# Performance work log

Measured on AMD Instinct MI355X. Metric: run time of the kernel, lower is better.

## Reference

```python
import jax, jax.numpy as jnp
import numpy as np

B, S, H = 4, 2048, 1024
NH = 16
D = H // NH
SCALE = 1.0 / np.sqrt(D).astype(np.float32)


def setup_inputs() -> dict:
    key = jax.random.key(0)
    ks = jax.random.split(key, 5)
    s = 1.0 / np.sqrt(H).astype(np.float32)  # ~ torch Linear init scale
    return {
        "x": jax.random.normal(ks[0], (B, S, H), jnp.float32),
        "Wq": jax.random.normal(ks[1], (H, H), jnp.float32) * s,
        "bq": jnp.zeros((H,), jnp.float32),
        "Wk": jax.random.normal(ks[2], (H, H), jnp.float32) * s,
        "bk": jnp.zeros((H,), jnp.float32),
        "Wv": jax.random.normal(ks[3], (H, H), jnp.float32) * s,
        "bv": jnp.zeros((H,), jnp.float32),
        "Wo": jax.random.normal(ks[4], (H, H), jnp.float32) * s,
        "bo": jnp.zeros((H,), jnp.float32),
    }


def reference(x, Wq, bq, Wk, bk, Wv, bv, Wo, bo):
    b, s, h = x.shape
    # qkv projections, split into heads: [b, nh, s, d]
    q = (x @ Wq.T + bq).reshape(b, s, NH, D).transpose(0, 2, 1, 3)
    k = (x @ Wk.T + bk).reshape(b, s, NH, D).transpose(0, 2, 1, 3)
    v = (x @ Wv.T + bv).reshape(b, s, NH, D).transpose(0, 2, 1, 3)
    att = jnp.einsum("bhqd,bhkd->bhqk", q, k) * SCALE
    att = jax.nn.softmax(att, axis=-1)  # stable max-subtract softmax
    # dropout(p=0.5) is identity in eval mode
    out = jnp.einsum("bhqk,bhkd->bhqd", att, v)
    out = out.transpose(0, 2, 1, 3).reshape(b, s, h)
    return out @ Wo.T + bo
```

## Files before the change

### kernel.cpp

```cpp
#include <hip/hip_runtime.h>
#include <hip/hip_bf16.h>
#include <stdint.h>
#include <math.h>

#define NB 4
#define NS 2048
#define NHID 1024
#define NHEAD 16
#define ND 64
#define NM (NB * NS)

typedef unsigned short u16;
typedef __attribute__((ext_vector_type(8))) short bf16x8;
typedef __attribute__((ext_vector_type(4))) float f32x4;

#define SC2F 0.18033688011112042f
#define DEFER_T 11.5416f


__device__ __forceinline__ u16 f2bf(float f) {
  union { float f; unsigned u; } v; v.f = f;
  unsigned u = v.u;
  return (u16)((u + 0x7FFFu + ((u >> 16) & 1u)) >> 16);
}

__device__ __forceinline__ void gload_lds16(const u16* g, u16* l) {
  __builtin_amdgcn_global_load_lds(
      (const __attribute__((address_space(1))) void*)g,
      (__attribute__((address_space(3))) void*)l, 16, 0, 0);
}

__device__ __forceinline__ f32x4 mfma16(bf16x8 a, bf16x8 b, f32x4 c) {
  return __builtin_amdgcn_mfma_f32_16x16x32_bf16(a, b, c, 0, 0, 0);
}

__device__ __forceinline__ unsigned cvtpk(float lo, float hi) {
  unsigned d;
  asm("v_cvt_pk_bf16_f32 %0, %1, %2" : "=v"(d) : "v"(lo), "v"(hi));
  return d;
}


__global__ __launch_bounds__(256) void convert_f32_bf16(
    const float* __restrict__ x, const float* __restrict__ wq,
    const float* __restrict__ wk, const float* __restrict__ wv,
    const float* __restrict__ wo,
    u16* __restrict__ xb, u16* __restrict__ wqb, u16* __restrict__ wkb,
    u16* __restrict__ wvb, u16* __restrict__ wob) {
  const float* src; u16* dst; int n;
  switch (blockIdx.y) {
    case 0:  src = x;  dst = xb;  n = NM * NHID;   break;
    case 1:  src = wq; dst = wqb; n = NHID * NHID; break;
    case 2:  src = wk; dst = wkb; n = NHID * NHID; break;
    case 3:  src = wv; dst = wvb; n = NHID * NHID; break;
    default: src = wo; dst = wob; n = NHID * NHID; break;
  }
  int stride = gridDim.x * blockDim.x * 4;
  for (int i = (blockIdx.x * blockDim.x + threadIdx.x) * 4; i < n; i += stride) {
    float4 v = *reinterpret_cast<const float4*>(src + i);
    ushort4 o;
    o.x = f2bf(v.x); o.y = f2bf(v.y); o.z = f2bf(v.z); o.w = f2bf(v.w);
    *reinterpret_cast<ushort4*>(dst + i) = o;
  }
}


__device__ __forceinline__ void gemm128_mainloop(
    const u16* __restrict__ A, const u16* __restrict__ Bw, int Kdim,
    int bm, int bn, u16* As, u16* Bs, f32x4 (&acc)[4][4]) {
  const int t = threadIdx.x;
  const int w = t >> 6;
  const int l = t & 63;
  const int lr = l & 15;
  const int kh = l >> 4;
  const int wr = w >> 1, wc = w & 1;

#pragma unroll
  for (int mi = 0; mi < 4; ++mi)
#pragma unroll
    for (int ni = 0; ni < 4; ++ni) acc[mi][ni] = (f32x4){0.f, 0.f, 0.f, 0.f};

  for (int k0 = 0; k0 < Kdim; k0 += 32) {
    __syncthreads();
#pragma unroll
    for (int j = 0; j < 2; ++j) {
      int idx = j * 256 + t;
      int row = idx >> 2;
      int kk  = (idx & 3) << 3;
      gload_lds16(A  + (size_t)(bm + row) * Kdim + k0 + kk, As + (size_t)(j * 256 + w * 64) * 8);
      gload_lds16(Bw + (size_t)(bn + row) * Kdim + k0 + kk, Bs + (size_t)(j * 256 + w * 64) * 8);
    }
    __syncthreads();

    bf16x8 af[4], bfr[4];
#pragma unroll
    for (int mi = 0; mi < 4; ++mi)
      af[mi] = *(const bf16x8*)&As[(wr * 64 + mi * 16 + lr) * 32 + kh * 8];
#pragma unroll
    for (int ni = 0; ni < 4; ++ni)
      bfr[ni] = *(const bf16x8*)&Bs[(wc * 64 + ni * 16 + lr) * 32 + kh * 8];
#pragma unroll
    for (int mi = 0; mi < 4; ++mi)
#pragma unroll
      for (int ni = 0; ni < 4; ++ni)
        acc[mi][ni] = mfma16(af[mi], bfr[ni], acc[mi][ni]);
  }
}


__global__ __launch_bounds__(256) void gemm_qkv(
    const u16* __restrict__ xb,
    const u16* __restrict__ wqb, const u16* __restrict__ wkb, const u16* __restrict__ wvb,
    const float* __restrict__ bq, const float* __restrict__ bk, const float* __restrict__ bv,
    u16* __restrict__ Qo, u16* __restrict__ Ko, u16* __restrict__ Vo) {
  __shared__ __align__(16) u16 As[128 * 32];
  __shared__ __align__(16) u16 Bs[128 * 32];
  const int which = blockIdx.z;
  const u16* Bw = (which == 0) ? wqb : (which == 1) ? wkb : wvb;
  const float* bias = (which == 0) ? bq : (which == 1) ? bk : bv;
  u16* outp = (which == 0) ? Qo : (which == 1) ? Ko : Vo;
  const int bm = blockIdx.x * 128, bn = blockIdx.y * 128;

  f32x4 acc[4][4];
  gemm128_mainloop(xb, Bw, NHID, bm, bn, As, Bs, acc);

  const int t = threadIdx.x, w = t >> 6, l = t & 63, lr = l & 15, hr = l >> 4;
  const int wr = w >> 1, wc = w & 1;
#pragma unroll
  for (int mi = 0; mi < 4; ++mi)
#pragma unroll
    for (int ni = 0; ni < 4; ++ni)
#pragma unroll
      for (int r = 0; r < 4; ++r) {
        int m = bm + wr * 64 + mi * 16 + hr * 4 + r;
        int n = bn + wc * 64 + ni * 16 + lr;
        float v = acc[mi][ni][r] + bias[n];
        if (which == 0) v *= SC2F;
        int b = m >> 11, s = m & (NS - 1), h = n >> 6, d = n & (ND - 1);
        size_t addr;
        if (which < 2) {
          addr = (((size_t)(b * NHEAD + h)) * NS + s) * ND + d;
        } else {
          int sp = (s & ~31) | (((s >> 2) & 3) * 8 + ((s >> 4) & 1) * 4 + (s & 3));
          addr = (((size_t)(b * NHEAD + h)) * ND + d) * NS + sp;
        }
        outp[addr] = f2bf(v);
      }
}


__global__ __launch_bounds__(256, 4) void attn_kernel(
    const u16* __restrict__ Q, const u16* __restrict__ K,
    const u16* __restrict__ Vt, u16* __restrict__ AO) {
  __shared__ __align__(16) u16 Ks[2][64 * 64];
  __shared__ __align__(16) u16 Vs[2][64 * 64];

  const int t = threadIdx.x, w = t >> 6, l = t & 63;
  const int lr = l & 15, g = l >> 4;
  const int bh = blockIdx.y;
  const int q0 = blockIdx.x * 128;

  const u16* Qh = Q  + (size_t)bh * NS * ND;
  const u16* Kh = K  + (size_t)bh * NS * ND;
  const u16* Vh = Vt + (size_t)bh * NS * ND;

  bf16x8 qf[2][2];
#pragma unroll
  for (int mi = 0; mi < 2; ++mi)
#pragma unroll
    for (int ks = 0; ks < 2; ++ks)
      qf[mi][ks] = *(const bf16x8*)(Qh + (size_t)(q0 + w * 32 + mi * 16 + lr) * ND + ks * 32 + g * 8);

  auto stage_kv = [&](int kt, int b) {
#pragma unroll
    for (int j = 0; j < 2; ++j) {
      int idx = j * 256 + t;
      int row = idx >> 3, sch = (idx & 7) ^ (row & 7);
      gload_lds16(Kh + (size_t)(kt + row) * ND + sch * 8, Ks[b] + (size_t)(j * 256 + w * 64) * 8);
      gload_lds16(Vh + (size_t)row * NS + kt + sch * 8,   Vs[b] + (size_t)(j * 256 + w * 64) * 8);
    }
  };

  stage_kv(0, 0);
  stage_kv(64, 1);

  f32x4 o[2][4];
  float m_i[2], l_i[2];
#pragma unroll
  for (int mi = 0; mi < 2; ++mi) {
#pragma unroll
    for (int ni = 0; ni < 4; ++ni) o[mi][ni] = (f32x4){0.f, 0.f, 0.f, 0.f};
    m_i[mi] = -INFINITY; l_i[mi] = 0.f;
  }

  const int nt = NS / 64;
  for (int ti = 0; ti < nt; ++ti) {
    const int b = ti & 1;
    if (ti == nt - 1) asm volatile("s_waitcnt vmcnt(0)" ::: "memory");
    else              asm volatile("s_waitcnt vmcnt(4)" ::: "memory");
    __builtin_amdgcn_s_barrier();

    f32x4 s[2][4];
#pragma unroll
    for (int mi = 0; mi < 2; ++mi)
#pragma unroll
      for (int ni = 0; ni < 4; ++ni) s[mi][ni] = (f32x4){0.f, 0.f, 0.f, 0.f};
    __builtin_amdgcn_s_setprio(1);
#pragma unroll
    for (int ks = 0; ks < 2; ++ks)
#pragma unroll
      for (int ni = 0; ni < 4; ++ni) {
        bf16x8 kf = *(const bf16x8*)&Ks[b][(ni * 16 + lr) * 64 + ((ks * 4 + g) ^ (lr & 7)) * 8];
        s[0][ni] = mfma16(kf, qf[0][ks], s[0][ni]);
        s[1][ni] = mfma16(kf, qf[1][ks], s[1][ni]);
      }
    __builtin_amdgcn_s_setprio(0);

    float pm[2];
#pragma unroll
    for (int mi = 0; mi < 2; ++mi) {
      float a0 = fmaxf(fmaxf(s[mi][0][0], s[mi][0][1]), fmaxf(s[mi][0][2], s[mi][0][3]));
      float a1 = fmaxf(fmaxf(s[mi][1][0], s[mi][1][1]), fmaxf(s[mi][1][2], s[mi][1][3]));
      float a2 = fmaxf(fmaxf(s[mi][2][0], s[mi][2][1]), fmaxf(s[mi][2][2], s[mi][2][3]));
      float a3 = fmaxf(fmaxf(s[mi][3][0], s[mi][3][1]), fmaxf(s[mi][3][2], s[mi][3][3]));
      pm[mi] = fmaxf(fmaxf(a0, a1), fmaxf(a2, a3));
      pm[mi] = fmaxf(pm[mi], __shfl_xor(pm[mi], 16, 64));
      pm[mi] = fmaxf(pm[mi], __shfl_xor(pm[mi], 32, 64));
    }

    bool ok = (pm[0] <= m_i[0] + DEFER_T) && (pm[1] <= m_i[1] + DEFER_T);
    if (!__all((int)ok)) {
      float sc[2];
#pragma unroll
      for (int mi = 0; mi < 2; ++mi) {
        float mn = fmaxf(m_i[mi], pm[mi]);
        sc[mi] = __builtin_amdgcn_exp2f(m_i[mi] - mn);
        m_i[mi] = mn;
        l_i[mi] *= sc[mi];
      }
#pragma unroll
      for (int mi = 0; mi < 2; ++mi)
#pragma unroll
        for (int r = 0; r < 4; ++r) {
          float so = __shfl(sc[mi], (l & 48) + g * 4 + r, 64);
#pragma unroll
          for (int ni = 0; ni < 4; ++ni) o[mi][ni][r] *= so;
        }
    }

#pragma unroll
    for (int mi = 0; mi < 2; ++mi) {
#pragma unroll
      for (int ni = 0; ni < 4; ++ni)
#pragma unroll
        for (int r = 0; r < 4; ++r)
          s[mi][ni][r] = __builtin_amdgcn_exp2f(s[mi][ni][r] - m_i[mi]);
      float b0 = (s[mi][0][0] + s[mi][0][1]) + (s[mi][0][2] + s[mi][0][3]);
      float b1 = (s[mi][1][0] + s[mi][1][1]) + (s[mi][1][2] + s[mi][1][3]);
      float b2 = (s[mi][2][0] + s[mi][2][1]) + (s[mi][2][2] + s[mi][2][3]);
      float b3 = (s[mi][3][0] + s[mi][3][1]) + (s[mi][3][2] + s[mi][3][3]);
      float rs = (b0 + b1) + (b2 + b3);
      rs += __shfl_xor(rs, 16, 64);
      rs += __shfl_xor(rs, 32, 64);
      l_i[mi] += rs;
    }

    __builtin_amdgcn_s_setprio(1);
#pragma unroll
    for (int ks = 0; ks < 2; ++ks) {
      union { bf16x8 v; unsigned u[4]; } pa0, pa1;
      pa0.u[0] = cvtpk(s[0][2 * ks][0], s[0][2 * ks][1]);
      pa0.u[1] = cvtpk(s[0][2 * ks][2], s[0][2 * ks][3]);
      pa0.u[2] = cvtpk(s[0][2 * ks + 1][0], s[0][2 * ks + 1][1]);
      pa0.u[3] = cvtpk(s[0][2 * ks + 1][2], s[0][2 * ks + 1][3]);
      pa1.u[0] = cvtpk(s[1][2 * ks][0], s[1][2 * ks][1]);
      pa1.u[1] = cvtpk(s[1][2 * ks][2], s[1][2 * ks][3]);
      pa1.u[2] = cvtpk(s[1][2 * ks + 1][0], s[1][2 * ks + 1][1]);
      pa1.u[3] = cvtpk(s[1][2 * ks + 1][2], s[1][2 * ks + 1][3]);
#pragma unroll
      for (int ni = 0; ni < 4; ++ni) {
        bf16x8 vf = *(const bf16x8*)&Vs[b][(ni * 16 + lr) * 64 + ((ks * 4 + g) ^ (lr & 7)) * 8];
        o[0][ni] = mfma16(pa0.v, vf, o[0][ni]);
        o[1][ni] = mfma16(pa1.v, vf, o[1][ni]);
      }
    }
    __builtin_amdgcn_s_setprio(0);

    asm volatile("s_waitcnt lgkmcnt(0)" ::: "memory");
    __builtin_amdgcn_s_barrier();
    if (ti + 2 < nt) stage_kv((ti + 2) * 64, b);
  }

  const int bb = bh >> 4, h = bh & (NHEAD - 1);
  float inv[2], invO[2][4];
#pragma unroll
  for (int mi = 0; mi < 2; ++mi) inv[mi] = 1.0f / l_i[mi];
#pragma unroll
  for (int mi = 0; mi < 2; ++mi)
#pragma unroll
    for (int r = 0; r < 4; ++r)
      invO[mi][r] = __shfl(inv[mi], (l & 48) + g * 4 + r, 64);
#pragma unroll
  for (int mi = 0; mi < 2; ++mi)
#pragma unroll
    for (int ni = 0; ni < 4; ++ni)
#pragma unroll
      for (int r = 0; r < 4; ++r) {
        int srow = q0 + w * 32 + mi * 16 + g * 4 + r;
        int col  = h * ND + ni * 16 + lr;
        AO[(size_t)(bb * NS + srow) * NHID + col] = f2bf(o[mi][ni][r] * invO[mi][r]);
      }
}


__global__ __launch_bounds__(256) void gemm_out(
    const u16* __restrict__ AO, const u16* __restrict__ wob,
    const float* __restrict__ bo, float* __restrict__ out) {
  __shared__ __align__(16) u16 As[128 * 32];
  __shared__ __align__(16) u16 Bs[128 * 32];
  const int bm = blockIdx.x * 128, bn = blockIdx.y * 128;

  f32x4 acc[4][4];
  gemm128_mainloop(AO, wob, NHID, bm, bn, As, Bs, acc);

  const int t = threadIdx.x, w = t >> 6, l = t & 63, lr = l & 15, hr = l >> 4;
  const int wr = w >> 1, wc = w & 1;
#pragma unroll
  for (int mi = 0; mi < 4; ++mi)
#pragma unroll
    for (int ni = 0; ni < 4; ++ni)
#pragma unroll
      for (int r = 0; r < 4; ++r) {
        int m = bm + wr * 64 + mi * 16 + hr * 4 + r;
        int n = bn + wc * 64 + ni * 16 + lr;
        out[(size_t)m * NHID + n] = acc[mi][ni][r] + bo[n];
      }
}


extern "C" void kernel_launch(void* const* d_in, const int* in_sizes, int n_in,
                              void* d_out, int out_size, void* d_ws, size_t ws_size,
                              hipStream_t stream) {
  const float* x  = (const float*)d_in[0];
  const float* Wq = (const float*)d_in[1];
  const float* bq = (const float*)d_in[2];
  const float* Wk = (const float*)d_in[3];
  const float* bk = (const float*)d_in[4];
  const float* Wv = (const float*)d_in[5];
  const float* bv = (const float*)d_in[6];
  const float* Wo = (const float*)d_in[7];
  const float* bo = (const float*)d_in[8];
  float* out = (float*)d_out;

  char* ws = (char*)d_ws;
  u16* xb  = (u16*)(ws + 0);
  u16* wqb = (u16*)(ws + 16777216);
  u16* wkb = (u16*)(ws + 18874368);
  u16* wvb = (u16*)(ws + 20971520);
  u16* wob = (u16*)(ws + 23068672);
  u16* Qb  = (u16*)(ws + 25165824);
  u16* Kb  = (u16*)(ws + 41943040);
  u16* Vtb = (u16*)(ws + 58720256);
  u16* AOb = (u16*)(ws + 75497472);

  convert_f32_bf16<<<dim3(512, 5), 256, 0, stream>>>(x, Wq, Wk, Wv, Wo, xb, wqb, wkb, wvb, wob);
  gemm_qkv<<<dim3(64, 8, 3), 256, 0, stream>>>(xb, wqb, wkb, wvb, bq, bk, bv, Qb, Kb, Vtb);
  attn_kernel<<<dim3(16, 64), 256, 0, stream>>>(Qb, Kb, Vtb, AOb);
  gemm_out<<<dim3(64, 8), 256, 0, stream>>>(AOb, wob, bo, out);
}
```

Before: 206.5 us.

## Double-buffer GEMM LDS tiles and simplify attention KV prefetch to one stage

The shared GEMM mainloop now uses two LDS buffers for A and B. The loads for the next K-slice are issued right after the barrier, so they overlap the MFMA work on the current slice, and one barrier per iteration is dropped. The attention kernel's KV staging goes from a two-tiles-ahead prefetch with hand-written vmcnt waits to a one-tile-ahead prefetch guarded by __syncthreads. This trades some latency hiding in attention for simpler synchronisation. LDS use in both GEMM kernels doubles.

```diff
diff --git a/kernel.cpp b/kernel.cpp
--- a/kernel.cpp
+++ b/kernel.cpp
@@ -67,7 +67,7 @@
 
 __device__ __forceinline__ void gemm128_mainloop(
     const u16* __restrict__ A, const u16* __restrict__ Bw, int Kdim,
-    int bm, int bn, u16* As, u16* Bs, f32x4 (&acc)[4][4]) {
+    int bm, int bn, u16 (*As)[128 * 32], u16 (*Bs)[128 * 32], f32x4 (&acc)[4][4]) {
   const int t = threadIdx.x;
   const int w = t >> 6;
   const int l = t & 63;
@@ -75,30 +75,39 @@
   const int kh = l >> 4;
   const int wr = w >> 1, wc = w & 1;
 
+  const int row0 = t >> 2,           kk0 = (t & 3) << 3;
+  const int row1 = (256 + t) >> 2,   kk1 = ((256 + t) & 3) << 3;
+  const u16* a0 = A  + (size_t)(bm + row0) * Kdim + kk0;
+  const u16* a1 = A  + (size_t)(bm + row1) * Kdim + kk1;
+  const u16* b0 = Bw + (size_t)(bn + row0) * Kdim + kk0;
+  const u16* b1 = Bw + (size_t)(bn + row1) * Kdim + kk1;
+
+  auto stage = [&](int k0, int buf) {
+    gload_lds16(a0 + k0, As[buf] + (size_t)(w * 64) * 8);
+    gload_lds16(b0 + k0, Bs[buf] + (size_t)(w * 64) * 8);
+    gload_lds16(a1 + k0, As[buf] + (size_t)(256 + w * 64) * 8);
+    gload_lds16(b1 + k0, Bs[buf] + (size_t)(256 + w * 64) * 8);
+  };
+
 #pragma unroll
   for (int mi = 0; mi < 4; ++mi)
 #pragma unroll
     for (int ni = 0; ni < 4; ++ni) acc[mi][ni] = (f32x4){0.f, 0.f, 0.f, 0.f};
 
-  for (int k0 = 0; k0 < Kdim; k0 += 32) {
+  stage(0, 0);
+  const int NK = Kdim / 32;
+  for (int kt = 0; kt < NK; ++kt) {
+    const int buf = kt & 1;
     __syncthreads();
-#pragma unroll
-    for (int j = 0; j < 2; ++j) {
-      int idx = j * 256 + t;
-      int row = idx >> 2;
-      int kk  = (idx & 3) << 3;
-      gload_lds16(A  + (size_t)(bm + row) * Kdim + k0 + kk, As + (size_t)(j * 256 + w * 64) * 8);
-      gload_lds16(Bw + (size_t)(bn + row) * Kdim + k0 + kk, Bs + (size_t)(j * 256 + w * 64) * 8);
-    }
-    __syncthreads();
+    if (kt + 1 < NK) stage((kt + 1) * 32, buf ^ 1);
 
     bf16x8 af[4], bfr[4];
 #pragma unroll
     for (int mi = 0; mi < 4; ++mi)
-      af[mi] = *(const bf16x8*)&As[(wr * 64 + mi * 16 + lr) * 32 + kh * 8];
+      af[mi] = *(const bf16x8*)&As[buf][(wr * 64 + mi * 16 + lr) * 32 + kh * 8];
 #pragma unroll
     for (int ni = 0; ni < 4; ++ni)
-      bfr[ni] = *(const bf16x8*)&Bs[(wc * 64 + ni * 16 + lr) * 32 + kh * 8];
+      bfr[ni] = *(const bf16x8*)&Bs[buf][(wc * 64 + ni * 16 + lr) * 32 + kh * 8];
 #pragma unroll
     for (int mi = 0; mi < 4; ++mi)
 #pragma unroll
@@ -113,8 +122,8 @@
     const u16* __restrict__ wqb, const u16* __restrict__ wkb, const u16* __restrict__ wvb,
     const float* __restrict__ bq, const float* __restrict__ bk, const float* __restrict__ bv,
     u16* __restrict__ Qo, u16* __restrict__ Ko, u16* __restrict__ Vo) {
-  __shared__ __align__(16) u16 As[128 * 32];
-  __shared__ __align__(16) u16 Bs[128 * 32];
+  __shared__ __align__(16) u16 As[2][128 * 32];
+  __shared__ __align__(16) u16 Bs[2][128 * 32];
   const int which = blockIdx.z;
   const u16* Bw = (which == 0) ? wqb : (which == 1) ? wkb : wvb;
   const float* bias = (which == 0) ? bq : (which == 1) ? bk : bv;
@@ -182,7 +191,6 @@
   };
 
   stage_kv(0, 0);
-  stage_kv(64, 1);
 
   f32x4 o[2][4];
   float m_i[2], l_i[2];
@@ -196,9 +204,8 @@
   const int nt = NS / 64;
   for (int ti = 0; ti < nt; ++ti) {
     const int b = ti & 1;
-    if (ti == nt - 1) asm volatile("s_waitcnt vmcnt(0)" ::: "memory");
-    else              asm volatile("s_waitcnt vmcnt(4)" ::: "memory");
-    __builtin_amdgcn_s_barrier();
+    __syncthreads();
+    if (ti + 1 < nt) stage_kv((ti + 1) * 64, b ^ 1);
 
     f32x4 s[2][4];
 #pragma unroll
@@ -285,10 +292,6 @@
       }
     }
     __builtin_amdgcn_s_setprio(0);
-
-    asm volatile("s_waitcnt lgkmcnt(0)" ::: "memory");
-    __builtin_amdgcn_s_barrier();
-    if (ti + 2 < nt) stage_kv((ti + 2) * 64, b);
   }
 
   const int bb = bh >> 4, h = bh & (NHEAD - 1);
@@ -316,8 +319,8 @@
 __global__ __launch_bounds__(256) void gemm_out(
     const u16* __restrict__ AO, const u16* __restrict__ wob,
     const float* __restrict__ bo, float* __restrict__ out) {
-  __shared__ __align__(16) u16 As[128 * 32];
-  __shared__ __align__(16) u16 Bs[128 * 32];
+  __shared__ __align__(16) u16 As[2][128 * 32];
+  __shared__ __align__(16) u16 Bs[2][128 * 32];
   const int bm = blockIdx.x * 128, bn = blockIdx.y * 128;
 
   f32x4 acc[4][4];
```

New measurement: 216.9 us. 5.0% more time.

## Use 256x128 triple-buffered swizzled GEMM tiles and simplify attention KV prefetch

Applied to the files above, without the earlier changes.

The QKV and output projection GEMMs move from a 128x128, K=32, single-buffered mainloop with two full barriers per step to a 256x128 tile. The new mainloop uses 512 threads, K=64 steps, a three-stage LDS ring with vmcnt-based waits and XOR-swizzled LDS layout, plus MFMA priority hints. This is meant to raise data reuse, hide global load latency and cut LDS bank conflicts. The attention kernel's two-tile-ahead KV prefetch with fine-grained waitcnts is replaced by a simpler one-ahead prefetch issued after a __syncthreads. That may reduce latency hiding in attention, and the 144KB LDS footprint limits GEMM occupancy to one block per CU.

```diff
diff --git a/kernel.cpp b/kernel.cpp
--- a/kernel.cpp
+++ b/kernel.cpp
@@ -65,75 +65,97 @@
 }
 
 
-__device__ __forceinline__ void gemm128_mainloop(
-    const u16* __restrict__ A, const u16* __restrict__ Bw, int Kdim,
-    int bm, int bn, u16* As, u16* Bs, f32x4 (&acc)[4][4]) {
+#define GNKT 16
+
+__device__ __forceinline__ void gemm256_mainloop(
+    const u16* __restrict__ A, const u16* __restrict__ Bw,
+    int bm, int bn, u16 (*lds)[24576], f32x4 (&acc)[4][4]) {
   const int t = threadIdx.x;
-  const int w = t >> 6;
-  const int l = t & 63;
-  const int lr = l & 15;
-  const int kh = l >> 4;
-  const int wr = w >> 1, wc = w & 1;
+  const int w = t >> 6, l = t & 63;
+  const int lr = l & 15, kh = l >> 4;
+  const int wm = w >> 1, wn = w & 1;
 
 #pragma unroll
   for (int mi = 0; mi < 4; ++mi)
 #pragma unroll
     for (int ni = 0; ni < 4; ++ni) acc[mi][ni] = (f32x4){0.f, 0.f, 0.f, 0.f};
 
-  for (int k0 = 0; k0 < Kdim; k0 += 32) {
-    __syncthreads();
-#pragma unroll
-    for (int j = 0; j < 2; ++j) {
-      int idx = j * 256 + t;
-      int row = idx >> 2;
-      int kk  = (idx & 3) << 3;
-      gload_lds16(A  + (size_t)(bm + row) * Kdim + k0 + kk, As + (size_t)(j * 256 + w * 64) * 8);
-      gload_lds16(Bw + (size_t)(bn + row) * Kdim + k0 + kk, Bs + (size_t)(j * 256 + w * 64) * 8);
-    }
-    __syncthreads();
-
-    bf16x8 af[4], bfr[4];
-#pragma unroll
-    for (int mi = 0; mi < 4; ++mi)
-      af[mi] = *(const bf16x8*)&As[(wr * 64 + mi * 16 + lr) * 32 + kh * 8];
-#pragma unroll
-    for (int ni = 0; ni < 4; ++ni)
-      bfr[ni] = *(const bf16x8*)&Bs[(wc * 64 + ni * 16 + lr) * 32 + kh * 8];
-#pragma unroll
-    for (int mi = 0; mi < 4; ++mi)
+  auto stage = [&](int kt, int buf) {
+    const int k0 = kt * 64;
+#pragma unroll
+    for (int it = 0; it < 4; ++it) {
+      int idx = it * 512 + t;
+      int row = idx >> 3, c = (idx & 7) ^ (row & 7);
+      gload_lds16(A + (size_t)(bm + row) * NHID + k0 + c * 8,
+                  lds[buf] + (size_t)(it * 512 + w * 64) * 8);
+    }
+#pragma unroll
+    for (int it = 0; it < 2; ++it) {
+      int idx = it * 512 + t;
+      int row = idx >> 3, c = (idx & 7) ^ (row & 7);
+      gload_lds16(Bw + (size_t)(bn + row) * NHID + k0 + c * 8,
+                  lds[buf] + 16384 + (size_t)(it * 512 + w * 64) * 8);
+    }
+  };
+
+  stage(0, 0);
+  stage(1, 1);
+
+  for (int kt = 0; kt < GNKT; ++kt) {
+    const int buf = kt % 3;
+    if (kt < GNKT - 1) asm volatile("s_waitcnt vmcnt(6)" ::: "memory");
+    else               asm volatile("s_waitcnt vmcnt(0)" ::: "memory");
+    __builtin_amdgcn_s_barrier();
+    if (kt + 2 < GNKT) stage(kt + 2, (kt + 2) % 3);
+
+    const u16* Ab = lds[buf];
+    const u16* Bb = lds[buf] + 16384;
+#pragma unroll
+    for (int ks = 0; ks < 2; ++ks) {
+      bf16x8 af[4], bfr[4];
+#pragma unroll
+      for (int mi = 0; mi < 4; ++mi)
+        af[mi] = *(const bf16x8*)&Ab[(wm * 64 + mi * 16 + lr) * 64 + (((ks * 4 + kh) ^ (lr & 7)) * 8)];
 #pragma unroll
       for (int ni = 0; ni < 4; ++ni)
-        acc[mi][ni] = mfma16(af[mi], bfr[ni], acc[mi][ni]);
-  }
-}
-
-
-__global__ __launch_bounds__(256) void gemm_qkv(
+        bfr[ni] = *(const bf16x8*)&Bb[(wn * 64 + ni * 16 + lr) * 64 + (((ks * 4 + kh) ^ (lr & 7)) * 8)];
+      __builtin_amdgcn_s_setprio(1);
+#pragma unroll
+      for (int mi = 0; mi < 4; ++mi)
+#pragma unroll
+        for (int ni = 0; ni < 4; ++ni)
+          acc[mi][ni] = mfma16(af[mi], bfr[ni], acc[mi][ni]);
+      __builtin_amdgcn_s_setprio(0);
+    }
+  }
+}
+
+
+__global__ __launch_bounds__(512, 2) void gemm_qkv(
     const u16* __restrict__ xb,
     const u16* __restrict__ wqb, const u16* __restrict__ wkb, const u16* __restrict__ wvb,
     const float* __restrict__ bq, const float* __restrict__ bk, const float* __restrict__ bv,
     u16* __restrict__ Qo, u16* __restrict__ Ko, u16* __restrict__ Vo) {
-  __shared__ __align__(16) u16 As[128 * 32];
-  __shared__ __align__(16) u16 Bs[128 * 32];
+  __shared__ __align__(16) u16 lds[3][24576];
   const int which = blockIdx.z;
   const u16* Bw = (which == 0) ? wqb : (which == 1) ? wkb : wvb;
   const float* bias = (which == 0) ? bq : (which == 1) ? bk : bv;
   u16* outp = (which == 0) ? Qo : (which == 1) ? Ko : Vo;
-  const int bm = blockIdx.x * 128, bn = blockIdx.y * 128;
+  const int bm = blockIdx.x * 256, bn = blockIdx.y * 128;
 
   f32x4 acc[4][4];
-  gemm128_mainloop(xb, Bw, NHID, bm, bn, As, Bs, acc);
-
-  const int t = threadIdx.x, w = t >> 6, l = t & 63, lr = l & 15, hr = l >> 4;
-  const int wr = w >> 1, wc = w & 1;
+  gemm256_mainloop(xb, Bw, bm, bn, lds, acc);
+
+  const int t = threadIdx.x, w = t >> 6, l = t & 63, lr = l & 15, kh = l >> 4;
+  const int wm = w >> 1, wn = w & 1;
 #pragma unroll
   for (int mi = 0; mi < 4; ++mi)
 #pragma unroll
     for (int ni = 0; ni < 4; ++ni)
 #pragma unroll
       for (int r = 0; r < 4; ++r) {
-        int m = bm + wr * 64 + mi * 16 + hr * 4 + r;
-        int n = bn + wc * 64 + ni * 16 + lr;
+        int m = bm + wm * 64 + mi * 16 + kh * 4 + r;
+        int n = bn + wn * 64 + ni * 16 + lr;
         float v = acc[mi][ni][r] + bias[n];
         if (which == 0) v *= SC2F;
         int b = m >> 11, s = m & (NS - 1), h = n >> 6, d = n & (ND - 1);
@@ -182,7 +204,6 @@
   };
 
   stage_kv(0, 0);
-  stage_kv(64, 1);
 
   f32x4 o[2][4];
   float m_i[2], l_i[2];
@@ -196,9 +217,8 @@
   const int nt = NS / 64;
   for (int ti = 0; ti < nt; ++ti) {
     const int b = ti & 1;
-    if (ti == nt - 1) asm volatile("s_waitcnt vmcnt(0)" ::: "memory");
-    else              asm volatile("s_waitcnt vmcnt(4)" ::: "memory");
-    __builtin_amdgcn_s_barrier();
+    __syncthreads();
+    if (ti + 1 < nt) stage_kv((ti + 1) * 64, b ^ 1);
 
     f32x4 s[2][4];
 #pragma unroll
@@ -285,10 +305,6 @@
       }
     }
     __builtin_amdgcn_s_setprio(0);
-
-    asm volatile("s_waitcnt lgkmcnt(0)" ::: "memory");
-    __builtin_amdgcn_s_barrier();
-    if (ti + 2 < nt) stage_kv((ti + 2) * 64, b);
   }
 
   const int bb = bh >> 4, h = bh & (NHEAD - 1);
@@ -313,26 +329,25 @@
 }
 
 
-__global__ __launch_bounds__(256) void gemm_out(
+__global__ __launch_bounds__(512, 2) void gemm_out(
     const u16* __restrict__ AO, const u16* __restrict__ wob,
     const float* __restrict__ bo, float* __restrict__ out) {
-  __shared__ __align__(16) u16 As[128 * 32];
-  __shared__ __align__(16) u16 Bs[128 * 32];
-  const int bm = blockIdx.x * 128, bn = blockIdx.y * 128;
+  __shared__ __align__(16) u16 lds[3][24576];
+  const int bm = blockIdx.x * 256, bn = blockIdx.y * 128;
 
   f32x4 acc[4][4];
-  gemm128_mainloop(AO, wob, NHID, bm, bn, As, Bs, acc);
-
-  const int t = threadIdx.x, w = t >> 6, l = t & 63, lr = l & 15, hr = l >> 4;
-  const int wr = w >> 1, wc = w & 1;
+  gemm256_mainloop(AO, wob, bm, bn, lds, acc);
+
+  const int t = threadIdx.x, w = t >> 6, l = t & 63, lr = l & 15, kh = l >> 4;
+  const int wm = w >> 1, wn = w & 1;
 #pragma unroll
   for (int mi = 0; mi < 4; ++mi)
 #pragma unroll
     for (int ni = 0; ni < 4; ++ni)
 #pragma unroll
       for (int r = 0; r < 4; ++r) {
-        int m = bm + wr * 64 + mi * 16 + hr * 4 + r;
-        int n = bn + wc * 64 + ni * 16 + lr;
+        int m = bm + wm * 64 + mi * 16 + kh * 4 + r;
+        int n = bn + wn * 64 + ni * 16 + lr;
         out[(size_t)m * NHID + n] = acc[mi][ni][r] + bo[n];
       }
 }
@@ -364,7 +379,7 @@
   u16* AOb = (u16*)(ws + 75497472);
 
   convert_f32_bf16<<<dim3(512, 5), 256, 0, stream>>>(x, Wq, Wk, Wv, Wo, xb, wqb, wkb, wvb, wob);
-  gemm_qkv<<<dim3(64, 8, 3), 256, 0, stream>>>(xb, wqb, wkb, wvb, bq, bk, bv, Qb, Kb, Vtb);
+  gemm_qkv<<<dim3(32, 8, 3), 512, 0, stream>>>(xb, wqb, wkb, wvb, bq, bk, bv, Qb, Kb, Vtb);
   attn_kernel<<<dim3(16, 64), 256, 0, stream>>>(Qb, Kb, Vtb, AOb);
-  gemm_out<<<dim3(64, 8), 256, 0, stream>>>(AOb, wob, bo, out);
-}
+  gemm_out<<<dim3(32, 8), 512, 0, stream>>>(AOb, wob, bo, out);
+}
```

New measurement: 196.2 us. 1.05x faster.
